# Kernel optimization log

Measured on AMD Instinct MI355X. Metric: run time of the kernel, lower is better.

The kernel has to match this reference:

```python
import jax, jax.numpy as jnp
import numpy as np
from jax import lax

B, L, V, D, NL, NH, DK, NT = 2, 2048, 10000, 50, 3, 4, 50, 22


def _sinusoid_table(n_position, d_hid):
    # faithful port of get_sinusoid_encoding_table (padding_idx=0 zeroed)
    pos = np.arange(n_position)[:, None].astype(np.float64)
    idx = np.arange(d_hid)[None, :]
    angle = pos / np.power(10000.0, 2 * (idx // 2) / d_hid)
    tab = np.zeros((n_position, d_hid))
    tab[:, 0::2] = np.sin(angle[:, 0::2])
    tab[:, 1::2] = np.cos(angle[:, 1::2])
    tab[0] = 0.0
    return jnp.asarray(tab, dtype=jnp.float32)


def _lstm(x, Wih, Whh, b):
    # torch nn.LSTM (batch_first), gate order i,f,g,o; b = b_ih + b_hh
    xw = x @ Wih.T + b  # [B,L,4H] input projection hoisted out of the scan
    Bsz = x.shape[0]
    H = Whh.shape[1]
    h0 = jnp.zeros((Bsz, H), x.dtype)
    c0 = jnp.zeros((Bsz, H), x.dtype)

    def step(carry, xt):
        h, c = carry
        g = xt + h @ Whh.T
        i, f, gg, o = jnp.split(g, 4, axis=-1)
        c = jax.nn.sigmoid(f) * c + jax.nn.sigmoid(i) * jnp.tanh(gg)
        h = jax.nn.sigmoid(o) * jnp.tanh(c)
        return (h, c), h

    _, hs = lax.scan(step, (h0, c0), xw.transpose(1, 0, 2))
    return hs.transpose(1, 0, 2)


def _layer_norm(x, g, b, eps=1e-5):
    m = x.mean(-1, keepdims=True)
    v = ((x - m) ** 2).mean(-1, keepdims=True)
    return (x - m) * lax.rsqrt(v + eps) * g + b


def _mha(xq, xkv, wq, bq, wk, bk, wv, bv, fcw, fcb, lng, lnb, mask):
    # MultiHeadAttention: bmm + scale + mask(-inf) + softmax + bmm,
    # then dropout(relu(fc(out))) [eval: dropout = identity], LN(out + residual)
    Bsz, Lq, _ = xq.shape
    Lk = xkv.shape[1]
    q = (xq @ wq + bq).reshape(Bsz, Lq, NH, DK)
    k = (xkv @ wk + bk).reshape(Bsz, Lk, NH, DK)
    v = (xkv @ wv + bv).reshape(Bsz, Lk, NH, DK)
    attn = jnp.einsum('bqhd,bkhd->bhqk', q, k) / jnp.sqrt(jnp.float32(DK))
    if mask is not None:
        # key-padding mask: True -> masked_fill(-inf)
        attn = jnp.where(mask[:, None, None, :], -jnp.inf, attn)
    a = jax.nn.softmax(attn, axis=-1)
    out = jnp.einsum('bhqk,bkhd->bqhd', a, v).reshape(Bsz, Lq, NH * DK)
    out = jax.nn.relu(out @ fcw + fcb)
    return _layer_norm(out + xq, lng, lnb)


def setup_inputs() -> dict:
    key = jax.random.key(0)
    ks = jax.random.split(key, 32)

    word_ids = jax.random.randint(ks[0], (B, L), 0, V, dtype=jnp.int32)
    lengths = jnp.array([L, L - 512], dtype=jnp.int32)  # exercise padding mask
    pad_mask = jnp.arange(L)[None, :] >= lengths[:, None]  # [B,L] True = pad

    word_emb = jax.random.normal(ks[1], (V, D), jnp.float32) * 0.1
    pos_emb = _sinusoid_table(L + 2, D)

    lstm_Wih = jax.random.normal(ks[2], (NL, 4 * D, D), jnp.float32) * 0.1
    lstm_Whh = jax.random.normal(ks[3], (NL, 4 * D, D), jnp.float32) * 0.1
    lstm_b = jnp.zeros((NL, 4 * D), jnp.float32)

    def mha_params(k0):
        kk = jax.random.split(k0, 4)
        return dict(
            wq=jax.random.normal(kk[0], (NL, D, NH * DK), jnp.float32) * np.sqrt(2.0 / (D + DK)),
            bq=jnp.zeros((NL, NH * DK), jnp.float32),
            wk=jax.random.normal(kk[1], (NL, D, NH * DK), jnp.float32) * np.sqrt(2.0 / (D + DK)),
            bk=jnp.zeros((NL, NH * DK), jnp.float32),
            wv=jax.random.normal(kk[2], (NL, D, NH * DK), jnp.float32) * np.sqrt(2.0 / (D + DK)),
            bv=jnp.zeros((NL, NH * DK), jnp.float32),
            fcw=jax.random.normal(kk[3], (NL, NH * DK, D), jnp.float32) * 0.07,
            fcb=jnp.zeros((NL, D), jnp.float32),
            lng=jnp.ones((NL, D), jnp.float32),
            lnb=jnp.zeros((NL, D), jnp.float32),
        )

    node = mha_params(ks[4])
    glo = mha_params(ks[5])

    tag_w = jax.random.normal(ks[6], (D, NT), jnp.float32) * 0.1
    tag_b = jnp.zeros((NT,), jnp.float32)

    inp = {'word_ids': word_ids, 'pad_mask': pad_mask,
           'word_emb': word_emb, 'pos_emb': pos_emb,
           'lstm_Wih': lstm_Wih, 'lstm_Whh': lstm_Whh, 'lstm_b': lstm_b}
    for pfx, p in (('node_', node), ('glo_', glo)):
        for n, v in p.items():
            inp[pfx + n] = v
    inp['tag_w'] = tag_w
    inp['tag_b'] = tag_b
    return inp


def reference(word_ids, pad_mask, word_emb, pos_emb, lstm_Wih, lstm_Whh, lstm_b,
              node_wq, node_bq, node_wk, node_bk, node_wv, node_bv,
              node_fcw, node_fcb, node_lng, node_lnb,
              glo_wq, glo_bq, glo_wk, glo_bk, glo_wv, glo_bv,
              glo_fcw, glo_fcb, glo_lng, glo_lnb, tag_w, tag_b):
    # embed + position (dropout is identity in eval)
    x = word_emb[word_ids] + pos_emb[jnp.arange(L) + 1][None]  # [B,L,D]
    for l in range(NL):
        h = _lstm(x, lstm_Wih[l], lstm_Whh[l], lstm_b[l])
        n = _mha(h, h, node_wq[l], node_bq[l], node_wk[l], node_bk[l],
                 node_wv[l], node_bv[l], node_fcw[l], node_fcb[l],
                 node_lng[l], node_lnb[l], pad_mask)
        x = _mha(n, n, glo_wq[l], glo_bq[l], glo_wk[l], glo_bk[l],
                 glo_wv[l], glo_bv[l], glo_fcw[l], glo_fcb[l],
                 glo_lng[l], glo_lnb[l], None)
    return x @ tag_w + tag_b  # [B,L,NT] emission scores for the CRF
```

## Files before the change

kernel.cpp:

```cpp
#include <hip/hip_runtime.h>
#include <hip/hip_bf16.h>


static constexpr int Bb  = 2;
static constexpr int Ls  = 2048;
static constexpr int Dd  = 50;
static constexpr int NLs = 3;
static constexpr int DKs = 50;
static constexpr int NTs = 22;
static constexpr int G4  = 200;
static constexpr int Ms  = Bb * Ls;
static constexpr int RS  = 52;

typedef float f2 __attribute__((ext_vector_type(2)));
typedef float f4 __attribute__((ext_vector_type(4)));

__device__ __forceinline__ void pkfma(f2& d, f2 a, f2 b) {
    asm("v_pk_fma_f32 %0, %1, %2, %0" : "+v"(d) : "v"(a), "v"(b));
}

__device__ __forceinline__ float sigm(float x) { return 1.f / (1.f + __expf(-x)); }
__device__ __forceinline__ float tanh_f(float x) { float e = __expf(2.f * x); return 1.f - 2.f / (e + 1.f); }

__device__ __forceinline__ void lds_barrier() {
    __builtin_amdgcn_sched_barrier(0);
    asm volatile("s_waitcnt lgkmcnt(0)" ::: "memory");
    __builtin_amdgcn_sched_barrier(0);
    __builtin_amdgcn_s_barrier();
    __builtin_amdgcn_sched_barrier(0);
}

__global__ __launch_bounds__(256) void k_embed(const int* __restrict__ ids,
                                               const float* __restrict__ wemb,
                                               const float* __restrict__ pemb,
                                               float* __restrict__ x) {
    int idx = blockIdx.x * 256 + threadIdx.x;
    if (idx >= Ms * Dd) return;
    int d = idx % Dd;
    int bl = idx / Dd;
    int l = bl % Ls;
    int w = ids[bl];
    x[idx] = wemb[w * Dd + d] + pemb[(l + 1) * Dd + d];
}

__global__ __launch_bounds__(256) void k_xw(const float* __restrict__ x,
                                            const float* __restrict__ W,
                                            const float* __restrict__ bias,
                                            float* __restrict__ y) {
    int idx = blockIdx.x * 256 + threadIdx.x;
    if (idx >= Ms * G4) return;
    int n = idx % G4;
    int m = idx / G4;
    const float* xr = x + m * Dd;
    const float* wr = W + n * Dd;
    float a0 = 0.f, a1 = 0.f;
#pragma unroll
    for (int k = 0; k < Dd; k += 2) {
        a0 += xr[k] * wr[k];
        a1 += xr[k + 1] * wr[k + 1];
    }
    y[idx] = a0 + a1 + bias[n];
}

__global__ __launch_bounds__(256, 1) void k_lstm(const float* __restrict__ xw,
                                                 const float* __restrict__ Whh,
                                                 float* __restrict__ hout) {
    int b = blockIdx.x;
    int w = threadIdx.x >> 6;
    int lane = threadIdx.x & 63;
    int e_loc = lane >> 2;
    int cch = lane & 3;
    int e = w * 13 + e_loc;
    bool act = (e_loc < 13) && (e < Dd);
    int ec = act ? e : (Dd - 1);
    int k0 = cch * 16;

    f2 wt[4][8];
#pragma unroll
    for (int g = 0; g < 4; ++g) {
        const float* wr = Whh + (size_t)(g * Dd + ec) * Dd;
#pragma unroll
        for (int p = 0; p < 8; ++p) {
            int kk = k0 + 2 * p;
            float lo = (kk < Dd) ? wr[kk] : 0.f;
            float hi = (kk + 1 < Dd) ? wr[kk + 1] : 0.f;
            wt[g][p] = f2{lo, hi};
        }
    }

    __shared__ __align__(16) float hS[2][64];
    if (threadIdx.x < 128) ((float*)hS)[threadIdx.x] = 0.f;
    float c = 0.f;
    const float* xwb = xw + (size_t)b * Ls * G4 + cch * Dd + ec;
    float xa = xwb[0], xb_ = xwb[(size_t)1 * G4], xc = xwb[(size_t)2 * G4],
          xd = xwb[(size_t)3 * G4];
    __syncthreads();

#define LSTM_STEP(PAR, XREG, TIDX)                                             \
    {                                                                          \
        const f4* h4 = (const f4*)(hS[PAR] + k0);                              \
        f4 h0 = h4[0], h1 = h4[1], h2v = h4[2], h3 = h4[3];                    \
        f2 hp[8] = {f2{h0.x, h0.y},   f2{h0.z, h0.w},   f2{h1.x, h1.y},        \
                    f2{h1.z, h1.w},   f2{h2v.x, h2v.y}, f2{h2v.z, h2v.w},      \
                    f2{h3.x, h3.y},   f2{h3.z, h3.w}};                         \
        f2 a0 = f2{0.f, 0.f}, a1 = f2{0.f, 0.f};                               \
        f2 a2 = f2{0.f, 0.f}, a3 = f2{0.f, 0.f};                               \
        _Pragma("unroll") for (int p = 0; p < 8; ++p) {                        \
            pkfma(a0, wt[0][p], hp[p]);                                        \
            pkfma(a1, wt[1][p], hp[p]);                                        \
            pkfma(a2, wt[2][p], hp[p]);                                        \
            pkfma(a3, wt[3][p], hp[p]);                                        \
        }                                                                      \
        float p0 = a0.x + a0.y, p1 = a1.x + a1.y;                              \
        float p2 = a2.x + a2.y, p3 = a3.x + a3.y;                              \
        float xcur = XREG;                                                     \
        p0 += (cch == 0) ? xcur : 0.f;                                         \
        p1 += (cch == 1) ? xcur : 0.f;                                         \
        p2 += (cch == 2) ? xcur : 0.f;                                         \
        p3 += (cch == 3) ? xcur : 0.f;                                         \
        if ((TIDX) + 4 < Ls) XREG = xwb[(size_t)((TIDX) + 4) * G4];            \
        p0 += __shfl_xor(p0, 1, 64); p1 += __shfl_xor(p1, 1, 64);              \
        p2 += __shfl_xor(p2, 1, 64); p3 += __shfl_xor(p3, 1, 64);              \
        p0 += __shfl_xor(p0, 2, 64); p1 += __shfl_xor(p1, 2, 64);              \
        p2 += __shfl_xor(p2, 2, 64); p3 += __shfl_xor(p3, 2, 64);              \
        c = sigm(p1) * c + sigm(p0) * tanh_f(p2);                              \
        float h = sigm(p3) * tanh_f(c);                                        \
        if (act && cch == 0) {                                                 \
            hS[(PAR) ^ 1][e] = h;                                              \
            hout[((size_t)b * Ls + (TIDX)) * Dd + e] = h;                      \
        }                                                                      \
        lds_barrier();                                                         \
    }

    for (int t = 0; t < Ls; t += 4) {
        LSTM_STEP(0, xa, t);
        LSTM_STEP(1, xb_, t + 1);
        LSTM_STEP(0, xc, t + 2);
        LSTM_STEP(1, xd, t + 3);
    }
#undef LSTM_STEP
}

__global__ __launch_bounds__(256) void k_qkv(const float* __restrict__ x,
                                             const float* __restrict__ wq,
                                             const float* __restrict__ bq,
                                             const float* __restrict__ wk,
                                             const float* __restrict__ bk,
                                             const float* __restrict__ wv,
                                             const float* __restrict__ bv,
                                             float* __restrict__ q, float* __restrict__ kk,
                                             float* __restrict__ v) {
    int idx = blockIdx.x * 256 + threadIdx.x;
    if (idx >= Ms * 3 * G4) return;
    int n = idx % G4;
    int t = (idx / G4) % 3;
    int m = idx / (3 * G4);
    const float* W = (t == 0) ? wq : ((t == 1) ? wk : wv);
    const float* Bi = (t == 0) ? bq : ((t == 1) ? bk : bv);
    const float* xr = x + m * Dd;
    float a0 = 0.f, a1 = 0.f;
#pragma unroll
    for (int k = 0; k < Dd; k += 2) {
        a0 += xr[k] * W[k * G4 + n];
        a1 += xr[k + 1] * W[(k + 1) * G4 + n];
    }
    float r = a0 + a1 + Bi[n];
    float* o = (t == 0) ? q : ((t == 1) ? kk : v);
    int head = n / Dd;
    int d = n - head * Dd;
    size_t base = ((size_t)head * Ms + m) * RS;
    o[base + d] = r;
    if (d == 0) { o[base + 50] = 0.f; o[base + 51] = 0.f; }
}

__global__ __launch_bounds__(256, 1) void k_attn(const float* __restrict__ q,
                                                 const float* __restrict__ k,
                                                 const float* __restrict__ v,
                                                 float* __restrict__ out, int use_mask) {
    __shared__ __align__(16) float lds[13824];

    int bid = blockIdx.x;
    int qblk = bid & 31;
    int head = (bid >> 5) & 3;
    int b = bid >> 7;
    int wave = threadIdx.x >> 6;
    int lane = threadIdx.x & 63;
    int row = qblk * 64 + lane;

    float* sK = lds + wave * 1664;
    float* sV = sK + 832;

    const float* qr = q + ((size_t)head * Ms + b * Ls + row) * RS;
    f2 q2[26];
    const f2* qp = (const f2*)qr;
#pragma unroll
    for (int p = 0; p < 26; ++p) q2[p] = qp[p];

    float m = -1e30f, lsum = 0.f;
    f2 acc2[26];
#pragma unroll
    for (int p = 0; p < 26; ++p) acc2[p] = f2{0.f, 0.f};

    int len = Ls;
    if (use_mask && b == 1) len = Ls - 512;
    int k0 = wave * 512;
    int ntile = 0;
    if (k0 < len) {
        int kend = (k0 + 512 < len) ? (k0 + 512) : len;
        ntile = (kend - k0) / 16;
    }

    int srow[4], sc4[4];
    bool sval[4];
#pragma unroll
    for (int i = 0; i < 4; ++i) {
        int g = lane + 64 * i;
        sval[i] = (g < 208);
        srow[i] = g / 13;
        sc4[i] = (g % 13) * 4;
    }
    const float* kb_ = k + ((size_t)head * Ms + b * Ls) * RS;
    const float* vb_ = v + ((size_t)head * Ms + b * Ls) * RS;

    f4 pk4[4], pv4[4];
    const float scl = 0.14142135623730950488f;

#define ISSUE(KT)                                                      \
    {                                                                  \
        _Pragma("unroll") for (int i = 0; i < 4; ++i) if (sval[i]) {   \
            size_t o = (size_t)((KT) + srow[i]) * RS + sc4[i];         \
            pk4[i] = *(const f4*)(kb_ + o);                            \
            pv4[i] = *(const f4*)(vb_ + o);                            \
        }                                                              \
    }
#define COMMIT()                                                       \
    {                                                                  \
        _Pragma("unroll") for (int i = 0; i < 4; ++i) if (sval[i]) {   \
            int lo = srow[i] * RS + sc4[i];                            \
            *(f4*)(sK + lo) = pk4[i];                                  \
            *(f4*)(sV + lo) = pv4[i];                                  \
        }                                                              \
    }

    if (ntile > 0) { ISSUE(k0); COMMIT(); }
    for (int t = 0; t < ntile; ++t) {
        bool pre = (t + 1 < ntile);
        if (pre) ISSUE(k0 + (t + 1) * 16);

        float s[16];
#pragma unroll
        for (int j = 0; j < 16; ++j) {
            f2 sj = f2{0.f, 0.f};
            const f4* kr4 = (const f4*)(sK + j * RS);
#pragma unroll
            for (int p = 0; p < 13; ++p) {
                f4 kv = kr4[p];
                pkfma(sj, q2[2 * p], f2{kv.x, kv.y});
                pkfma(sj, q2[2 * p + 1], f2{kv.z, kv.w});
            }
            s[j] = (sj.x + sj.y) * scl;
        }
        float cm = s[0];
#pragma unroll
        for (int j = 1; j < 16; ++j) cm = fmaxf(cm, s[j]);
        float mn = fmaxf(m, cm);
        float corr = __expf(m - mn);
        lsum *= corr;
#pragma unroll
        for (int p = 0; p < 26; ++p) { acc2[p].x *= corr; acc2[p].y *= corr; }
#pragma unroll
        for (int j = 0; j < 16; ++j) {
            float pj = __expf(s[j] - mn);
            lsum += pj;
            f2 p2 = f2{pj, pj};
            const f4* vr4 = (const f4*)(sV + j * RS);
#pragma unroll
            for (int p = 0; p < 13; ++p) {
                f4 vv = vr4[p];
                pkfma(acc2[2 * p], p2, f2{vv.x, vv.y});
                pkfma(acc2[2 * p + 1], p2, f2{vv.z, vv.w});
            }
        }
        m = mn;
        if (pre) COMMIT();
    }
#undef ISSUE
#undef COMMIT

    __syncthreads();
    float* lmS = lds;
    float* llS = lds + 256;
    float* lacc = lds + 512;
    lmS[wave * 64 + lane] = m;
    llS[wave * 64 + lane] = lsum;
    float* la = lacc + (wave * 64 + lane) * RS;
#pragma unroll
    for (int p = 0; p < 26; ++p) { la[2 * p] = acc2[p].x; la[2 * p + 1] = acc2[p].y; }
    __syncthreads();

    for (int idx = threadIdx.x; idx < 64 * DKs; idx += 256) {
        int r = idx / DKs;
        int d = idx - r * DKs;
        float M = fmaxf(fmaxf(lmS[r], lmS[64 + r]), fmaxf(lmS[128 + r], lmS[192 + r]));
        float Lt = 0.f, val = 0.f;
#pragma unroll
        for (int w2 = 0; w2 < 4; ++w2) {
            float wg = __expf(lmS[w2 * 64 + r] - M);
            Lt += wg * llS[w2 * 64 + r];
            val += wg * lacc[(w2 * 64 + r) * RS + d];
        }
        out[((size_t)head * Ms + b * Ls + qblk * 64 + r) * RS + d] = val / Lt;
    }
}

__global__ __launch_bounds__(64) void k_fcln(const float* __restrict__ ao,
                                             const float* __restrict__ fcw,
                                             const float* __restrict__ fcb,
                                             const float* __restrict__ lng,
                                             const float* __restrict__ lnb,
                                             const float* __restrict__ resid,
                                             float* __restrict__ out) {
    int row = blockIdx.x;
    int lane = threadIdx.x;
    float acc = 0.f;
    if (lane < Dd) {
        float a0 = 0.f, a1 = 0.f;
#pragma unroll
        for (int hd = 0; hd < 4; ++hd) {
            const float* ar = ao + ((size_t)hd * Ms + row) * RS;
            const float* wr = fcw + hd * Dd * Dd;
#pragma unroll
            for (int kk = 0; kk < Dd; kk += 2) {
                a0 += ar[kk] * wr[kk * Dd + lane];
                a1 += ar[kk + 1] * wr[(kk + 1) * Dd + lane];
            }
        }
        acc = a0 + a1 + fcb[lane];
        acc = fmaxf(acc, 0.f);
        acc += resid[(size_t)row * Dd + lane];
    }
    float s = (lane < Dd) ? acc : 0.f;
#pragma unroll
    for (int off = 32; off; off >>= 1) s += __shfl_xor(s, off, 64);
    float mean = s / (float)Dd;
    float dv = (lane < Dd) ? (acc - mean) : 0.f;
    float s2 = dv * dv;
#pragma unroll
    for (int off = 32; off; off >>= 1) s2 += __shfl_xor(s2, off, 64);
    float var = s2 / (float)Dd;
    if (lane < Dd) {
        float r = (acc - mean) * rsqrtf(var + 1e-5f) * lng[lane] + lnb[lane];
        out[(size_t)row * Dd + lane] = r;
    }
}

__global__ __launch_bounds__(256) void k_tag(const float* __restrict__ x,
                                             const float* __restrict__ tw,
                                             const float* __restrict__ tb,
                                             float* __restrict__ out) {
    int idx = blockIdx.x * 256 + threadIdx.x;
    if (idx >= Ms * NTs) return;
    int n = idx % NTs;
    int m = idx / NTs;
    const float* xr = x + m * Dd;
    float a0 = 0.f, a1 = 0.f;
#pragma unroll
    for (int k = 0; k < Dd; k += 2) {
        a0 += xr[k] * tw[k * NTs + n];
        a1 += xr[k + 1] * tw[(k + 1) * NTs + n];
    }
    out[idx] = a0 + a1 + tb[n];
}

extern "C" void kernel_launch(void* const* d_in, const int* in_sizes, int n_in,
                              void* d_out, int out_size, void* d_ws, size_t ws_size,
                              hipStream_t stream) {
    const int* ids = (const int*)d_in[0];
    const float* wemb = (const float*)d_in[2];
    const float* pemb = (const float*)d_in[3];
    const float* Wih = (const float*)d_in[4];
    const float* Whh = (const float*)d_in[5];
    const float* lb = (const float*)d_in[6];
    const float* n_wq = (const float*)d_in[7];
    const float* n_bq = (const float*)d_in[8];
    const float* n_wk = (const float*)d_in[9];
    const float* n_bk = (const float*)d_in[10];
    const float* n_wv = (const float*)d_in[11];
    const float* n_bv = (const float*)d_in[12];
    const float* n_fcw = (const float*)d_in[13];
    const float* n_fcb = (const float*)d_in[14];
    const float* n_lng = (const float*)d_in[15];
    const float* n_lnb = (const float*)d_in[16];
    const float* g_wq = (const float*)d_in[17];
    const float* g_bq = (const float*)d_in[18];
    const float* g_wk = (const float*)d_in[19];
    const float* g_bk = (const float*)d_in[20];
    const float* g_wv = (const float*)d_in[21];
    const float* g_bv = (const float*)d_in[22];
    const float* g_fcw = (const float*)d_in[23];
    const float* g_fcb = (const float*)d_in[24];
    const float* g_lng = (const float*)d_in[25];
    const float* g_lnb = (const float*)d_in[26];
    const float* tw = (const float*)d_in[27];
    const float* tb = (const float*)d_in[28];

    const int MD = Ms * Dd;
    const int MG = Ms * G4;
    const int MH = 4 * Ms * RS;
    float* ws = (float*)d_ws;
    float* x = ws;
    float* xwb = x + MD;
    float* hb = xwb + MG;
    float* qb = hb + MD;
    float* kb = qb + MH;
    float* vb = kb + MH;
    float* aob = vb + MH;
    float* nb = aob + MH;

    k_embed<<<(MD + 255) / 256, 256, 0, stream>>>(ids, wemb, pemb, x);

    for (int l = 0; l < NLs; ++l) {
        const int wOff = l * G4 * Dd;
        const int b4Off = l * G4;
        const int dOff = l * Dd;

        k_xw<<<(MG + 255) / 256, 256, 0, stream>>>(x, Wih + wOff, lb + b4Off, xwb);
        k_lstm<<<Bb, 256, 0, stream>>>(xwb, Whh + wOff, hb);

        k_qkv<<<(3 * MG + 255) / 256, 256, 0, stream>>>(hb, n_wq + wOff, n_bq + b4Off,
                                                        n_wk + wOff, n_bk + b4Off,
                                                        n_wv + wOff, n_bv + b4Off, qb, kb, vb);
        k_attn<<<256, 256, 0, stream>>>(qb, kb, vb, aob, 1);
        k_fcln<<<Ms, 64, 0, stream>>>(aob, n_fcw + wOff, n_fcb + dOff, n_lng + dOff,
                                      n_lnb + dOff, hb, nb);

        k_qkv<<<(3 * MG + 255) / 256, 256, 0, stream>>>(nb, g_wq + wOff, g_bq + b4Off,
                                                        g_wk + wOff, g_bk + b4Off,
                                                        g_wv + wOff, g_bv + b4Off, qb, kb, vb);
        k_attn<<<256, 256, 0, stream>>>(qb, kb, vb, aob, 0);
        k_fcln<<<Ms, 64, 0, stream>>>(aob, g_fcw + wOff, g_fcb + dOff, g_lng + dOff,
                                      g_lnb + dOff, nb, x);
    }

    k_tag<<<(Ms * NTs + 255) / 256, 256, 0, stream>>>(x, tw, tb, (float*)d_out);
}
```

Measured before the change: 4.496 ms.

## Split attention key range across two blocks and merge partials in a new kernel

The attention kernel now splits each query block's key range into two halves handled by separate blocks, doubling the grid so that more CUs, and more waves per CU, are active. Each block writes a normalized partial output in bf16 together with its running max and sum. A new merge kernel then combines the two partials with log-sum-exp weighting. This costs an extra launch, extra global traffic and a loss of precision from the bf16 partials, and the partial buffers reuse the front of the workspace that holds x and xwb.

```diff
diff --git a/kernel.cpp b/kernel.cpp
--- a/kernel.cpp
+++ b/kernel.cpp
@@ -11,6 +11,7 @@
 static constexpr int G4  = 200;
 static constexpr int Ms  = Bb * Ls;
 static constexpr int RS  = 52;
+static constexpr int PS  = 56;
 
 typedef float f2 __attribute__((ext_vector_type(2)));
 typedef float f4 __attribute__((ext_vector_type(4)));
@@ -173,16 +174,20 @@
     if (d == 0) { o[base + 50] = 0.f; o[base + 51] = 0.f; }
 }
 
-__global__ __launch_bounds__(256, 1) void k_attn(const float* __restrict__ q,
-                                                 const float* __restrict__ k,
-                                                 const float* __restrict__ v,
-                                                 float* __restrict__ out, int use_mask) {
+__global__ __launch_bounds__(256, 1) void k_attn2(const float* __restrict__ q,
+                                                  const float* __restrict__ k,
+                                                  const float* __restrict__ v,
+                                                  __hip_bfloat16* __restrict__ pv,
+                                                  float* __restrict__ pml,
+                                                  int use_mask) {
     __shared__ __align__(16) float lds[13824];
 
     int bid = blockIdx.x;
-    int qblk = bid & 31;
-    int head = (bid >> 5) & 3;
-    int b = bid >> 7;
+    int s = bid >> 8;
+    int inner = bid & 255;
+    int qblk = inner & 31;
+    int head = (inner >> 5) & 3;
+    int b = inner >> 7;
     int wave = threadIdx.x >> 6;
     int lane = threadIdx.x & 63;
     int row = qblk * 64 + lane;
@@ -203,10 +208,10 @@
 
     int len = Ls;
     if (use_mask && b == 1) len = Ls - 512;
-    int k0 = wave * 512;
+    int k0 = s * 1024 + wave * 256;
     int ntile = 0;
     if (k0 < len) {
-        int kend = (k0 + 512 < len) ? (k0 + 512) : len;
+        int kend = (k0 + 256 < len) ? (k0 + 256) : len;
         ntile = (kend - k0) / 16;
     }
 
@@ -247,7 +252,7 @@
         bool pre = (t + 1 < ntile);
         if (pre) ISSUE(k0 + (t + 1) * 16);
 
-        float s[16];
+        float sc[16];
 #pragma unroll
         for (int j = 0; j < 16; ++j) {
             f2 sj = f2{0.f, 0.f};
@@ -258,11 +263,11 @@
                 pkfma(sj, q2[2 * p], f2{kv.x, kv.y});
                 pkfma(sj, q2[2 * p + 1], f2{kv.z, kv.w});
             }
-            s[j] = (sj.x + sj.y) * scl;
+            sc[j] = (sj.x + sj.y) * scl;
         }
-        float cm = s[0];
-#pragma unroll
-        for (int j = 1; j < 16; ++j) cm = fmaxf(cm, s[j]);
+        float cm = sc[0];
+#pragma unroll
+        for (int j = 1; j < 16; ++j) cm = fmaxf(cm, sc[j]);
         float mn = fmaxf(m, cm);
         float corr = __expf(m - mn);
         lsum *= corr;
@@ -270,7 +275,7 @@
         for (int p = 0; p < 26; ++p) { acc2[p].x *= corr; acc2[p].y *= corr; }
 #pragma unroll
         for (int j = 0; j < 16; ++j) {
-            float pj = __expf(s[j] - mn);
+            float pj = __expf(sc[j] - mn);
             lsum += pj;
             f2 p2 = f2{pj, pj};
             const f4* vr4 = (const f4*)(sV + j * RS);
@@ -298,6 +303,7 @@
     for (int p = 0; p < 26; ++p) { la[2 * p] = acc2[p].x; la[2 * p + 1] = acc2[p].y; }
     __syncthreads();
 
+    size_t pbase = (((size_t)s * 4 + head) * Ms + b * Ls + qblk * 64);
     for (int idx = threadIdx.x; idx < 64 * DKs; idx += 256) {
         int r = idx / DKs;
         int d = idx - r * DKs;
@@ -309,7 +315,41 @@
             Lt += wg * llS[w2 * 64 + r];
             val += wg * lacc[(w2 * 64 + r) * RS + d];
         }
-        out[((size_t)head * Ms + b * Ls + qblk * 64 + r) * RS + d] = val / Lt;
+        pv[(pbase + r) * PS + d] = __float2bfloat16(val / Lt);
+    }
+    if (threadIdx.x < 64) {
+        int r = threadIdx.x;
+        float M = fmaxf(fmaxf(lmS[r], lmS[64 + r]), fmaxf(lmS[128 + r], lmS[192 + r]));
+        float Lt = 0.f;
+#pragma unroll
+        for (int w2 = 0; w2 < 4; ++w2)
+            Lt += __expf(lmS[w2 * 64 + r] - M) * llS[w2 * 64 + r];
+        pml[(pbase + r) * 2] = M;
+        pml[(pbase + r) * 2 + 1] = Lt;
+    }
+}
+
+__global__ __launch_bounds__(256) void k_merge(const __hip_bfloat16* __restrict__ pv,
+                                               const float* __restrict__ pml,
+                                               float* __restrict__ out) {
+    int inner = blockIdx.x;
+    int qblk = inner & 31;
+    int head = (inner >> 5) & 3;
+    int b = inner >> 7;
+    size_t rowbase = (size_t)b * Ls + qblk * 64;
+    for (int idx = threadIdx.x; idx < 64 * DKs; idx += 256) {
+        int r = idx / DKs;
+        int d = idx - r * DKs;
+        size_t r0 = ((size_t)head * Ms + rowbase + r);
+        size_t r1 = ((size_t)(4 + head) * Ms + rowbase + r);
+        float m0 = pml[r0 * 2], l0 = pml[r0 * 2 + 1];
+        float m1 = pml[r1 * 2], l1 = pml[r1 * 2 + 1];
+        float Mg = fmaxf(m0, m1);
+        float w0 = __expf(m0 - Mg) * l0;
+        float w1 = __expf(m1 - Mg) * l1;
+        float v0 = __bfloat162float(pv[r0 * PS + d]);
+        float v1 = __bfloat162float(pv[r1 * PS + d]);
+        out[((size_t)head * Ms + rowbase + r) * RS + d] = (w0 * v0 + w1 * v1) / (w0 + w1);
     }
 }
 
@@ -417,6 +457,9 @@
     float* aob = vb + MH;
     float* nb = aob + MH;
 
+    __hip_bfloat16* pvS = (__hip_bfloat16*)ws;
+    float* pmlS = (float*)((char*)ws + (size_t)2 * 4 * Ms * PS * 2);
+
     k_embed<<<(MD + 255) / 256, 256, 0, stream>>>(ids, wemb, pemb, x);
 
     for (int l = 0; l < NLs; ++l) {
@@ -430,14 +473,16 @@
         k_qkv<<<(3 * MG + 255) / 256, 256, 0, stream>>>(hb, n_wq + wOff, n_bq + b4Off,
                                                         n_wk + wOff, n_bk + b4Off,
                                                         n_wv + wOff, n_bv + b4Off, qb, kb, vb);
-        k_attn<<<256, 256, 0, stream>>>(qb, kb, vb, aob, 1);
+        k_attn2<<<512, 256, 0, stream>>>(qb, kb, vb, pvS, pmlS, 1);
+        k_merge<<<256, 256, 0, stream>>>(pvS, pmlS, aob);
         k_fcln<<<Ms, 64, 0, stream>>>(aob, n_fcw + wOff, n_fcb + dOff, n_lng + dOff,
                                       n_lnb + dOff, hb, nb);
 
         k_qkv<<<(3 * MG + 255) / 256, 256, 0, stream>>>(nb, g_wq + wOff, g_bq + b4Off,
                                                         g_wk + wOff, g_bk + b4Off,
                                                         g_wv + wOff, g_bv + b4Off, qb, kb, vb);
-        k_attn<<<256, 256, 0, stream>>>(qb, kb, vb, aob, 0);
+        k_attn2<<<512, 256, 0, stream>>>(qb, kb, vb, pvS, pmlS, 0);
+        k_merge<<<256, 256, 0, stream>>>(pvS, pmlS, aob);
         k_fcln<<<Ms, 64, 0, stream>>>(aob, g_fcw + wOff, g_fcb + dOff, g_lng + dOff,
                                       g_lnb + dOff, nb, x);
     }
```

Measured after the change: 4.084 ms. -9.2%, faster.
